# Optimization experiments

Measured on AMD Instinct MI355X. Metric: run time of the kernel, lower is better.

Reference implementation:

```python
import jax, jax.numpy as jnp
import numpy as np
from jax import lax

TARGETED_NUM_POINTS = 2000


def fps_indices(pts, m):
    """Furthest-point sampling indices for one cloud. pts: [n,3] -> [m] int32.
    Matches pointnet2_utils.furthest_point_sample: first index is 0, then
    iteratively pick the point with max distance to the selected set."""
    n = pts.shape[0]

    def step(carry, _):
        dist, last = carry
        d = jnp.sum((pts - pts[last]) ** 2, axis=-1)  # [n]
        dist = jnp.minimum(dist, d)
        nxt = jnp.argmax(dist).astype(jnp.int32)
        return (dist, nxt), nxt

    dist0 = jnp.full((n,), 1e10, dtype=pts.dtype)
    (_, _), idxs = lax.scan(step, (dist0, jnp.int32(0)), None, length=m - 1)
    return jnp.concatenate([jnp.zeros((1,), jnp.int32), idxs])


def setup_inputs() -> dict:
    key = jax.random.key(0)
    k1, k2 = jax.random.split(key)
    batch, n_pts, c = 8, 20000, 128
    return {
        "input_C": jax.random.normal(k1, (batch * n_pts, 3), dtype=jnp.float32),
        "input_F": jax.random.normal(k2, (batch * n_pts, c), dtype=jnp.float32),
        "batch": batch,
        "n_pts": n_pts,
    }


def reference(input_C, input_F, batch, n_pts):
    # pts_list = [n_pts]*batch (equal-size clouds), so the flat tensors reshape cleanly.
    C = input_C.reshape(batch, n_pts, 3)
    F = input_F.reshape(batch, n_pts, -1)
    m = min(TARGETED_NUM_POINTS, n_pts)
    idxs = jax.vmap(lambda p: fps_indices(p, m))(C)  # [b, m]
    sampled_C = jnp.take_along_axis(C, idxs[..., None], axis=1)  # [b, m, 3]
    sampled_F = jnp.take_along_axis(F, idxs[..., None], axis=1)  # [b, m, c]
    return sampled_C, sampled_F
```

## Files before the change

### kernel.cpp

```cpp
#include <hip/hip_runtime.h>
#include <hip/hip_bf16.h>

typedef unsigned long long ull;

#define THREADS 1024
#define NWAVE 16

template<int CTRL, int RM>
__device__ __forceinline__ float fmax_dpp(float v) {
    int s = __builtin_amdgcn_update_dpp(__float_as_int(v), __float_as_int(v), CTRL, RM, 0xf, false);
    return fmaxf(v, __int_as_float(s));
}
template<int CTRL, int RM>
__device__ __forceinline__ float fmin_dpp(float v) {
    int s = __builtin_amdgcn_update_dpp(__float_as_int(v), __float_as_int(v), CTRL, RM, 0xf, false);
    return fminf(v, __int_as_float(s));
}
template<int CTRL, int RM>
__device__ __forceinline__ int imin_dpp(int v) {
    int s = __builtin_amdgcn_update_dpp(v, v, CTRL, RM, 0xf, false);
    return (s < v) ? s : v;
}
template<int CTRL, int RM>
__device__ __forceinline__ ull kmax_dpp(ull k) {
    unsigned hi = (unsigned)(k >> 32), lo = (unsigned)k;
    unsigned hi2 = (unsigned)__builtin_amdgcn_update_dpp((int)hi, (int)hi, CTRL, RM, 0xf, false);
    unsigned lo2 = (unsigned)__builtin_amdgcn_update_dpp((int)lo, (int)lo, CTRL, RM, 0xf, false);
    ull k2 = ((ull)hi2 << 32) | lo2;
    return (k2 > k) ? k2 : k;
}
__device__ __forceinline__ float wave_fmax(float v) {
    v = fmax_dpp<0x111,0xf>(v); v = fmax_dpp<0x112,0xf>(v);
    v = fmax_dpp<0x114,0xf>(v); v = fmax_dpp<0x118,0xf>(v);
    v = fmax_dpp<0x142,0xa>(v); v = fmax_dpp<0x143,0xc>(v);
    return v;
}
__device__ __forceinline__ float wave_fmin(float v) {
    v = fmin_dpp<0x111,0xf>(v); v = fmin_dpp<0x112,0xf>(v);
    v = fmin_dpp<0x114,0xf>(v); v = fmin_dpp<0x118,0xf>(v);
    v = fmin_dpp<0x142,0xa>(v); v = fmin_dpp<0x143,0xc>(v);
    return v;
}
__device__ __forceinline__ float half_fmax(float v) {
    v = fmax_dpp<0x111,0xf>(v); v = fmax_dpp<0x112,0xf>(v);
    v = fmax_dpp<0x114,0xf>(v); v = fmax_dpp<0x118,0xf>(v);
    v = fmax_dpp<0x142,0xa>(v);
    return v;
}
__device__ __forceinline__ float half_fmin(float v) {
    v = fmin_dpp<0x111,0xf>(v); v = fmin_dpp<0x112,0xf>(v);
    v = fmin_dpp<0x114,0xf>(v); v = fmin_dpp<0x118,0xf>(v);
    v = fmin_dpp<0x142,0xa>(v);
    return v;
}
__device__ __forceinline__ int half_imin(int v) {
    v = imin_dpp<0x111,0xf>(v); v = imin_dpp<0x112,0xf>(v);
    v = imin_dpp<0x114,0xf>(v); v = imin_dpp<0x118,0xf>(v);
    v = imin_dpp<0x142,0xa>(v);
    return v;
}
__device__ __forceinline__ ull wave_kmax(ull k) {
    k = kmax_dpp<0x111,0xf>(k); k = kmax_dpp<0x112,0xf>(k);
    k = kmax_dpp<0x114,0xf>(k); k = kmax_dpp<0x118,0xf>(k);
    k = kmax_dpp<0x142,0xa>(k); k = kmax_dpp<0x143,0xc>(k);
    return k;
}
__device__ __forceinline__ int morton4(int x, int y, int z) {
    int r = 0;
#pragma unroll
    for (int k = 0; k < 4; ++k)
        r |= ((x >> k & 1) << (3 * k)) | ((y >> k & 1) << (3 * k + 1)) | ((z >> k & 1) << (3 * k + 2));
    return r;
}
__device__ __forceinline__ int cellof(float x, float y, float z,
                                      float bx, float by, float bz,
                                      float ivx, float ivy, float ivz) {
    int ix = (int)((x - bx) * ivx); ix = ix < 0 ? 0 : (ix > 15 ? 15 : ix);
    int iy = (int)((y - by) * ivy); iy = iy < 0 ? 0 : (iy > 15 ? 15 : iy);
    int iz = (int)((z - bz) * ivz); iz = iz < 0 ? 0 : (iz > 15 ? 15 : iz);
    return morton4(ix, iy, iz);
}

#define OFS_GKEY 0
#define OFS_GMAX 8192
#define OFS_CX   12288
#define OFS_CY   16384
#define OFS_CZ   20480
#define OFS_EX   24576
#define OFS_EY   28672
#define OFS_EZ   32768
#define OFS_LIST 36864
#define OFS_PART 38912
#define OFS_MISC 39168
#define OFS_RED  39296
#define FIXED_BYTES 39680

__global__ __launch_bounds__(THREADS)
void fps_grouped(const float* __restrict__ C, float4* __restrict__ gxyzo,
                 int n, int m, int G32, int* __restrict__ idx_out) {
    const int b = blockIdx.x;
    const int t = threadIdx.x;
    const int lane = t & 63;
    const int wid  = t >> 6;
    const int half = lane >> 5;
    const int sub  = lane & 31;
    const int GP = G32 * 32;
    const float* __restrict__ P = C + (size_t)b * n * 3;
    float4* __restrict__ gx = gxyzo + (size_t)b * GP;

    extern __shared__ char smem[];
    ull*   s_gkey = (ull*)(smem + OFS_GKEY);
    float* s_gmax = (float*)(smem + OFS_GMAX);
    float* s_cx   = (float*)(smem + OFS_CX);
    float* s_cy   = (float*)(smem + OFS_CY);
    float* s_cz   = (float*)(smem + OFS_CZ);
    float* s_ex   = (float*)(smem + OFS_EX);
    float* s_ey   = (float*)(smem + OFS_EY);
    float* s_ez   = (float*)(smem + OFS_EZ);
    unsigned short* s_list = (unsigned short*)(smem + OFS_LIST);
    ull*   s_part = (ull*)(smem + OFS_PART);
    int*   s_misc = (int*)(smem + OFS_MISC);
    float* s_red  = (float*)(smem + OFS_RED);
    float* s_dist = (float*)(smem + FIXED_BYTES);
    unsigned* s_hist = (unsigned*)s_dist;

    float mnx = 1e30f, mny = 1e30f, mnz = 1e30f;
    float mxx = -1e30f, mxy = -1e30f, mxz = -1e30f;
    for (int g = t; g < n; g += THREADS) {
        float x = P[3 * g], y = P[3 * g + 1], z = P[3 * g + 2];
        mnx = fminf(mnx, x); mxx = fmaxf(mxx, x);
        mny = fminf(mny, y); mxy = fmaxf(mxy, y);
        mnz = fminf(mnz, z); mxz = fmaxf(mxz, z);
    }
    mnx = wave_fmin(mnx); mny = wave_fmin(mny); mnz = wave_fmin(mnz);
    mxx = wave_fmax(mxx); mxy = wave_fmax(mxy); mxz = wave_fmax(mxz);
    if (lane == 63) {
        s_red[wid * 6 + 0] = mnx; s_red[wid * 6 + 1] = mny; s_red[wid * 6 + 2] = mnz;
        s_red[wid * 6 + 3] = mxx; s_red[wid * 6 + 4] = mxy; s_red[wid * 6 + 5] = mxz;
    }
    __syncthreads();
    if (t == 0) {
        float a0 = 1e30f, a1 = 1e30f, a2 = 1e30f, b0 = -1e30f, b1 = -1e30f, b2 = -1e30f;
        for (int w = 0; w < NWAVE; ++w) {
            a0 = fminf(a0, s_red[w * 6 + 0]); a1 = fminf(a1, s_red[w * 6 + 1]);
            a2 = fminf(a2, s_red[w * 6 + 2]); b0 = fmaxf(b0, s_red[w * 6 + 3]);
            b1 = fmaxf(b1, s_red[w * 6 + 4]); b2 = fmaxf(b2, s_red[w * 6 + 5]);
        }
        s_red[0] = a0; s_red[1] = a1; s_red[2] = a2;
        s_red[3] = 15.9999f / (b0 - a0 + 1e-20f);
        s_red[4] = 15.9999f / (b1 - a1 + 1e-20f);
        s_red[5] = 15.9999f / (b2 - a2 + 1e-20f);
    }
    __syncthreads();
    const float bx = s_red[0], by = s_red[1], bz = s_red[2];
    const float ivx = s_red[3], ivy = s_red[4], ivz = s_red[5];

    for (int i = t; i < 4096; i += THREADS) s_hist[i] = 0;
    __syncthreads();
    for (int g = t; g < n; g += THREADS) {
        float x = P[3 * g], y = P[3 * g + 1], z = P[3 * g + 2];
        atomicAdd(&s_hist[cellof(x, y, z, bx, by, bz, ivx, ivy, ivz)], 1u);
    }
    __syncthreads();

    {
        unsigned c0 = s_hist[4 * t], c1 = s_hist[4 * t + 1];
        unsigned c2 = s_hist[4 * t + 2], c3 = s_hist[4 * t + 3];
        unsigned sum4 = c0 + c1 + c2 + c3;
        unsigned incl = sum4;
        for (int off = 1; off < 64; off <<= 1) {
            unsigned u = (unsigned)__shfl_up((int)incl, off);
            if (lane >= off) incl += u;
        }
        if (lane == 63) s_misc[8 + wid] = (int)incl;
        __syncthreads();
        unsigned woff = 0;
        for (int w = 0; w < wid; ++w) woff += (unsigned)s_misc[8 + w];
        unsigned base = woff + incl - sum4;
        s_hist[4 * t]     = base;
        s_hist[4 * t + 1] = base + c0;
        s_hist[4 * t + 2] = base + c0 + c1;
        s_hist[4 * t + 3] = base + c0 + c1 + c2;
    }
    __syncthreads();

    for (int g = t; g < n; g += THREADS) {
        float x = P[3 * g], y = P[3 * g + 1], z = P[3 * g + 2];
        unsigned pos = atomicAdd(&s_hist[cellof(x, y, z, bx, by, bz, ivx, ivy, ivz)], 1u);
        gx[pos] = make_float4(x, y, z, (float)g);
    }
    __syncthreads();

    const ull BIGKEY = ((ull)__float_as_uint(1e10f) << 15) | 0x7fffULL;
    for (int g = wid; g < G32; g += NWAVE) {
        int cnt = n - g * 32; if (cnt > 32) cnt = 32;
        bool memb = (lane < 32) && (sub < cnt);
        float4 w = make_float4(0.f, 0.f, 0.f, 0.f);
        if (memb) w = gx[g * 32 + sub];
        float xn = memb ? w.x : 1e30f, xx = memb ? w.x : -1e30f;
        float yn = memb ? w.y : 1e30f, yx = memb ? w.y : -1e30f;
        float zn = memb ? w.z : 1e30f, zx = memb ? w.z : -1e30f;
        xn = __shfl(half_fmin(xn), 31); xx = __shfl(half_fmax(xx), 31);
        yn = __shfl(half_fmin(yn), 31); yx = __shfl(half_fmax(yx), 31);
        zn = __shfl(half_fmin(zn), 31); zx = __shfl(half_fmax(zx), 31);
        if (lane == 0) {
            s_cx[g] = (xn + xx) * 0.5f; s_ex[g] = (xx - xn) * 0.5f + 1e-7f;
            s_cy[g] = (yn + yx) * 0.5f; s_ey[g] = (yx - yn) * 0.5f + 1e-7f;
            s_cz[g] = (zn + zx) * 0.5f; s_ez[g] = (zx - zn) * 0.5f + 1e-7f;
            s_gmax[g] = 1e10f;
            s_gkey[g] = BIGKEY;
        }
        if (lane < 32) {
            if (!memb) gx[g * 32 + sub] = make_float4(0.f, 0.f, 0.f, 0.f);
            s_dist[g * 32 + sub] = memb ? 1e10f : -1.0f;
        }
    }
    for (int i = t; i < 1024; i += THREADS)
        if (i >= G32) s_gkey[i] = 0;
    if (t == 0) { s_misc[0] = 0; idx_out[(size_t)b * m] = 0; }
    __syncthreads();

    float lx = P[0], ly = P[1], lz = P[2];
    const size_t iobase = (size_t)b * m;
    const int DW = (G32 + 63) >> 6;
    for (int it = 1; it < m; ++it) {
        const int par = (it & 1) * 16;

        bool upd = false;
        if (t < G32) {
            float gmax = s_gmax[t];
            float ax = fmaxf(fabsf(lx - s_cx[t]) - s_ex[t], 0.0f);
            float ay = fmaxf(fabsf(ly - s_cy[t]) - s_ey[t], 0.0f);
            float az = fmaxf(fabsf(lz - s_cz[t]) - s_ez[t], 0.0f);
            float lb2 = ax * ax + ay * ay + az * az;
            upd = !(lb2 * 0.9999f - 1e-6f >= gmax);
        }
        {
            ull mask = __ballot(upd);
            if (mask) {
                int cnt = __popcll(mask);
                int base = 0;
                if (lane == 0) base = atomicAdd(&s_misc[0], cnt);
                base = __shfl(base, 0);
                if (upd) {
                    int pw = (int)__popcll(mask & ((1ULL << lane) - 1ULL));
                    s_list[base + pw] = (unsigned short)t;
                }
            }
        }
        __syncthreads();
        const int U = s_misc[0];

        {
            const int nt = (U + 1) >> 1;
            for (int j0 = wid; j0 < nt; j0 += NWAVE) {
                int e = 2 * j0 + half;
                int g = (e < U) ? (int)s_list[e] : -1;
                int o = g * 32 + sub;
                float4 w = make_float4(0.f, 0.f, 0.f, 0.f);
                float dc = -1.0f;
                if (g >= 0) { w = gx[o]; dc = s_dist[o]; }
                float dx = __fsub_rn(w.x, lx);
                float dy = __fsub_rn(w.y, ly);
                float dz = __fsub_rn(w.z, lz);
                float d  = __fadd_rn(__fadd_rn(__fmul_rn(dx, dx), __fmul_rn(dy, dy)),
                                     __fmul_rn(dz, dz));
                float nd = fminf(dc, d);
                if (g >= 0) s_dist[o] = nd;
                float gmr = nd;
                gmr = fmax_dpp<0x111,0xf>(gmr);
                gmr = fmax_dpp<0x112,0xf>(gmr);
                gmr = fmax_dpp<0x114,0xf>(gmr);
                gmr = fmax_dpp<0x118,0xf>(gmr);
                gmr = fmax_dpp<0x142,0xa>(gmr);
                float gm = __shfl(gmr, lane | 31);
                ull mask = __ballot(nd == gm);
                unsigned hm = half ? (unsigned)(mask >> 32) : (unsigned)mask;
                int fl = __ffs((int)hm) - 1;
                int ao = __shfl((int)w.w, (half << 5) + fl);
                bool tie = (hm & (hm - 1u)) != 0u;
                if (__any(tie)) {
                    int morig = (nd == gm) ? (int)w.w : 0x7FFFFFFF;
                    morig = half_imin(morig);
                    int tmin = __shfl(morig, lane | 31);
                    if (tie) ao = tmin;
                }
                if (g >= 0 && sub == 31) {
                    s_gkey[g] = ((ull)__float_as_uint(gm) << 15)
                              | (ull)(unsigned)(0x7fff - ao);
                    s_gmax[g] = gm;
                }
            }
        }
        __syncthreads();

        ull kk = 0;
        if (wid < DW) kk = wave_kmax(s_gkey[t]);
        if (lane == 63) s_part[par + wid] = kk;
        if (t == 0) s_misc[0] = 0;
        __syncthreads();
        ull k2 = s_part[par + (t & 15)];
        k2 = kmax_dpp<0x111,0xf>(k2);
        k2 = kmax_dpp<0x112,0xf>(k2);
        k2 = kmax_dpp<0x114,0xf>(k2);
        k2 = kmax_dpp<0x118,0xf>(k2);
        int lo15 = __builtin_amdgcn_readlane((int)(unsigned)k2, 15);
        int orig = 0x7fff - (lo15 & 0x7fff);
        if (t == 0) idx_out[iobase + it] = orig;
        const float* __restrict__ wp = P + 3 * (size_t)orig;
        lx = wp[0]; ly = wp[1]; lz = wp[2];
    }
}

__global__ __launch_bounds__(1024)
void fps_brute(const float* __restrict__ C, float* __restrict__ gdist,
               int n, int m, int* __restrict__ idx_out) {
    const int b = blockIdx.x, t = threadIdx.x;
    const int lane = t & 63, wid = t >> 6;
    const float* __restrict__ P = C + (size_t)b * n * 3;
    float* __restrict__ dist = gdist + (size_t)b * n;
    __shared__ ull sp[2][16];
    for (int g = t; g < n; g += 1024) dist[g] = 1e10f;
    if (t == 0) idx_out[(size_t)b * m] = 0;
    float lx = P[0], ly = P[1], lz = P[2];
    __syncthreads();
    for (int it = 1; it < m; ++it) {
        int par = it & 1;
        ull k = 0;
        for (int g = t; g < n; g += 1024) {
            float dx = __fsub_rn(P[3 * g], lx);
            float dy = __fsub_rn(P[3 * g + 1], ly);
            float dz = __fsub_rn(P[3 * g + 2], lz);
            float d = __fadd_rn(__fadd_rn(__fmul_rn(dx, dx), __fmul_rn(dy, dy)),
                                __fmul_rn(dz, dz));
            float nd = fminf(dist[g], d);
            dist[g] = nd;
            ull kk = ((ull)__float_as_uint(nd) << 32) | (unsigned)(~g);
            if (kk > k) k = kk;
        }
        for (int off = 1; off < 64; off <<= 1) {
            ull ok = __shfl_xor(k, off);
            if (ok > k) k = ok;
        }
        if (lane == 0) sp[par][wid] = k;
        __syncthreads();
        ull kmaxv = sp[par][0];
        for (int w = 1; w < 16; ++w) { ull v = sp[par][w]; if (v > kmaxv) kmaxv = v; }
        int sbi = (int)~(unsigned)kmaxv;
        if (t == 0) idx_out[(size_t)b * m + it] = sbi;
        const float* wp = P + 3 * (size_t)(unsigned)sbi;
        lx = wp[0]; ly = wp[1]; lz = wp[2];
    }
}

__global__ void gather_kernel(const float* __restrict__ C,
                              const float* __restrict__ F,
                              const int* __restrict__ idx,
                              float* __restrict__ outC,
                              float* __restrict__ outF,
                              int n_pts, int m, int c) {
    int pair = blockIdx.x;
    int b = pair / m;
    int src = idx[pair];
    size_t srcbase = (size_t)b * n_pts + src;
    const float* sF = F + srcbase * (size_t)c;
    float* dF = outF + (size_t)pair * c;
    for (int i = threadIdx.x; i < c; i += blockDim.x) dF[i] = sF[i];
    if (threadIdx.x < 3)
        outC[(size_t)pair * 3 + threadIdx.x] = C[srcbase * 3 + threadIdx.x];
}

extern "C" void kernel_launch(void* const* d_in, const int* in_sizes, int n_in,
                              void* d_out, int out_size, void* d_ws, size_t ws_size,
                              hipStream_t stream) {
    const float* C = (const float*)d_in[0];
    const float* F = (const float*)d_in[1];

    int n_total = in_sizes[0] / 3;
    int c       = in_sizes[1] / n_total;
    int bm      = out_size / (3 + c);

    int batch = 8;
    if (bm % 2000 == 0) {
        int bb = bm / 2000;
        if (bb > 0 && n_total % bb == 0 && n_total / bb >= 2000) batch = bb;
    }
    int n_pts = n_total / batch;
    int m     = (n_pts < 2000) ? n_pts : 2000;

    int* idxbuf = (int*)d_ws;
    float* outC = (float*)d_out;
    float* outF = outC + (size_t)batch * m * 3;

    int G32 = (n_pts + 31) >> 5;
    int GP  = G32 << 5;
    size_t idxbytes = (((size_t)batch * m * 4) + 255) & ~(size_t)255;
    size_t scrbytes = (size_t)batch * GP * 16;
    void* scratch;
    if (ws_size >= idxbytes + scrbytes)
        scratch = (char*)d_ws + idxbytes;
    else
        scratch = (char*)d_out + ((((size_t)out_size * 4) - scrbytes) & ~(size_t)15);

    if (n_pts <= 32767) {
        int distbytes = GP * 4; if (distbytes < 16384) distbytes = 16384;
        size_t smem = (size_t)FIXED_BYTES + distbytes;
        hipFuncSetAttribute((const void*)fps_grouped,
                            hipFuncAttributeMaxDynamicSharedMemorySize, (int)smem);
        fps_grouped<<<batch, THREADS, smem, stream>>>(C, (float4*)scratch,
                                                      n_pts, m, G32, idxbuf);
    } else {
        fps_brute<<<batch, 1024, 0, stream>>>(C, (float*)scratch, n_pts, m, idxbuf);
    }

    gather_kernel<<<batch * m, 128, 0, stream>>>(C, F, idxbuf, outC, outF,
                                                 n_pts, m, c);
}
```

Measured before the change: 3.094 ms.

## Replace block-level argmax reduction with redundant per-wave scan and unroll phase C

Every wave now scans all group keys in shared memory and reduces redundantly, which removes the two-stage partial-max step and one block barrier per iteration. The candidate list is double-buffered so its counter can be reset without an extra barrier. The per-group distance update loop is unrolled four ways so that global loads are batched. The iteration is reordered to run an initial full update before the loop, and the final update is skipped. In exchange, each wave does more redundant LDS reads (G32/64 per lane), and the unrolled loop raises register pressure.

```diff
diff --git a/kernel.cpp b/kernel.cpp
--- a/kernel.cpp
+++ b/kernel.cpp
@@ -81,19 +81,88 @@
     return morton4(ix, iy, iz);
 }
 
-#define OFS_GKEY 0
-#define OFS_GMAX 8192
-#define OFS_CX   12288
-#define OFS_CY   16384
-#define OFS_CZ   20480
-#define OFS_EX   24576
-#define OFS_EY   28672
-#define OFS_EZ   32768
-#define OFS_LIST 36864
-#define OFS_PART 38912
-#define OFS_MISC 39168
-#define OFS_RED  39296
-#define FIXED_BYTES 39680
+#define OFS_GKEY  0
+#define OFS_GMAX  8192
+#define OFS_CX    12288
+#define OFS_CY    16384
+#define OFS_CZ    20480
+#define OFS_EX    24576
+#define OFS_EY    28672
+#define OFS_EZ    32768
+#define OFS_LIST0 36864
+#define OFS_LIST1 38912
+#define OFS_MISC  40960
+#define OFS_RED   41088
+#define FIXED_BYTES 41472
+
+__device__ __forceinline__ void phaseC(
+    const float4* __restrict__ gx, float* __restrict__ s_dist,
+    ull* __restrict__ s_gkey, float* __restrict__ s_gmax,
+    const unsigned short* __restrict__ lst, int U,
+    int lane, int half, int sub, int wid,
+    float lx, float ly, float lz)
+{
+    const int nt = (U + 1) >> 1;
+    for (int j = wid; j < nt; j += 4 * NWAVE) {
+        const int j1 = j + NWAVE, j2 = j + 2 * NWAVE, j3 = j + 3 * NWAVE;
+        int e0 = 2 * j  + half, e1 = 2 * j1 + half;
+        int e2 = 2 * j2 + half, e3 = 2 * j3 + half;
+        bool a0 = e0 < U;
+        bool a1 = (j1 < nt) && (e1 < U);
+        bool a2 = (j2 < nt) && (e2 < U);
+        bool a3 = (j3 < nt) && (e3 < U);
+        int g0 = lst[a0 ? e0 : 0], g1 = lst[a1 ? e1 : 0];
+        int g2 = lst[a2 ? e2 : 0], g3 = lst[a3 ? e3 : 0];
+        int o0 = g0 * 32 + sub, o1 = g1 * 32 + sub;
+        int o2 = g2 * 32 + sub, o3 = g3 * 32 + sub;
+        float4 w0 = gx[o0];
+        float4 w1 = gx[o1];
+        float4 w2 = gx[o2];
+        float4 w3 = gx[o3];
+        float d0 = s_dist[o0], d1 = s_dist[o1];
+        float d2 = s_dist[o2], d3 = s_dist[o3];
+
+#define PROC(W, DC, G, O, VALID)                                              \
+        {                                                                     \
+            float dx = __fsub_rn(W.x, lx);                                    \
+            float dy = __fsub_rn(W.y, ly);                                    \
+            float dz = __fsub_rn(W.z, lz);                                    \
+            float d  = __fadd_rn(__fadd_rn(__fmul_rn(dx, dx),                 \
+                                           __fmul_rn(dy, dy)),               \
+                                 __fmul_rn(dz, dz));                          \
+            float nd = fminf(DC, d);                                          \
+            if (VALID) s_dist[O] = nd;                                        \
+            float gmr = nd;                                                   \
+            gmr = fmax_dpp<0x111,0xf>(gmr);                                   \
+            gmr = fmax_dpp<0x112,0xf>(gmr);                                   \
+            gmr = fmax_dpp<0x114,0xf>(gmr);                                   \
+            gmr = fmax_dpp<0x118,0xf>(gmr);                                   \
+            gmr = fmax_dpp<0x142,0xa>(gmr);                                   \
+            float gm = __shfl(gmr, lane | 31);                                \
+            ull mask = __ballot(nd == gm);                                    \
+            unsigned hm = half ? (unsigned)(mask >> 32) : (unsigned)mask;     \
+            int fl = __ffs((int)hm) - 1;                                      \
+            int ao = __shfl((int)W.w, (half << 5) + fl);                      \
+            bool tie = (hm & (hm - 1u)) != 0u;                                \
+            if (__any(tie)) {                                                 \
+                int morig = (nd == gm) ? (int)W.w : 0x7FFFFFFF;               \
+                morig = half_imin(morig);                                     \
+                int tmin = __shfl(morig, lane | 31);                          \
+                if (tie) ao = tmin;                                           \
+            }                                                                 \
+            if (VALID && sub == 31) {                                         \
+                s_gkey[G] = ((ull)__float_as_uint(gm) << 15)                  \
+                          | (ull)(unsigned)(0x7fff - ao);                     \
+                s_gmax[G] = gm;                                               \
+            }                                                                 \
+        }
+        PROC(w0, d0, g0, o0, a0)
+        PROC(w1, d1, g1, o1, a1)
+        PROC(w2, d2, g2, o2, a2)
+        PROC(w3, d3, g3, o3, a3)
+#undef PROC
+    }
+}
 
 __global__ __launch_bounds__(THREADS)
 void fps_grouped(const float* __restrict__ C, float4* __restrict__ gxyzo,
@@ -117,8 +186,8 @@
     float* s_ex   = (float*)(smem + OFS_EX);
     float* s_ey   = (float*)(smem + OFS_EY);
     float* s_ez   = (float*)(smem + OFS_EZ);
-    unsigned short* s_list = (unsigned short*)(smem + OFS_LIST);
-    ull*   s_part = (ull*)(smem + OFS_PART);
+    unsigned short* s_list0 = (unsigned short*)(smem + OFS_LIST0);
+    unsigned short* s_list1 = (unsigned short*)(smem + OFS_LIST1);
     int*   s_misc = (int*)(smem + OFS_MISC);
     float* s_red  = (float*)(smem + OFS_RED);
     float* s_dist = (float*)(smem + FIXED_BYTES);
@@ -191,7 +260,6 @@
     }
     __syncthreads();
 
-    const ull BIGKEY = ((ull)__float_as_uint(1e10f) << 15) | 0x7fffULL;
     for (int g = wid; g < G32; g += NWAVE) {
         int cnt = n - g * 32; if (cnt > 32) cnt = 32;
         bool memb = (lane < 32) && (sub < cnt);
@@ -207,24 +275,36 @@
             s_cx[g] = (xn + xx) * 0.5f; s_ex[g] = (xx - xn) * 0.5f + 1e-7f;
             s_cy[g] = (yn + yx) * 0.5f; s_ey[g] = (yx - yn) * 0.5f + 1e-7f;
             s_cz[g] = (zn + zx) * 0.5f; s_ez[g] = (zx - zn) * 0.5f + 1e-7f;
-            s_gmax[g] = 1e10f;
-            s_gkey[g] = BIGKEY;
         }
         if (lane < 32) {
             if (!memb) gx[g * 32 + sub] = make_float4(0.f, 0.f, 0.f, 0.f);
             s_dist[g * 32 + sub] = memb ? 1e10f : -1.0f;
         }
     }
-    for (int i = t; i < 1024; i += THREADS)
-        if (i >= G32) s_gkey[i] = 0;
-    if (t == 0) { s_misc[0] = 0; idx_out[(size_t)b * m] = 0; }
+    for (int i = t; i < G32; i += THREADS) s_list0[i] = (unsigned short)i;
+    if (t == 0) { s_misc[0] = G32; s_misc[1] = 0; idx_out[(size_t)b * m] = 0; }
     __syncthreads();
 
     float lx = P[0], ly = P[1], lz = P[2];
     const size_t iobase = (size_t)b * m;
-    const int DW = (G32 + 63) >> 6;
+    phaseC(gx, s_dist, s_gkey, s_gmax, s_list0, G32, lane, half, sub, wid, lx, ly, lz);
+    __syncthreads();
+
     for (int it = 1; it < m; ++it) {
-        const int par = (it & 1) * 16;
+        const int p = it & 1;
+
+        ull kb = 0;
+        for (int k = lane; k < G32; k += 64) {
+            ull v = s_gkey[k];
+            if (v > kb) kb = v;
+        }
+        kb = wave_kmax(kb);
+        unsigned klo = (unsigned)__builtin_amdgcn_readlane((int)(unsigned)kb, 63);
+        int orig = 0x7fff - (int)(klo & 0x7fffu);
+        if (t == 0) idx_out[iobase + it] = orig;
+        if (it == m - 1) break;
+        const float* __restrict__ wp = P + 3 * (size_t)orig;
+        lx = wp[0]; ly = wp[1]; lz = wp[2];
 
         bool upd = false;
         if (t < G32) {
@@ -235,80 +315,26 @@
             float lb2 = ax * ax + ay * ay + az * az;
             upd = !(lb2 * 0.9999f - 1e-6f >= gmax);
         }
+        if (t == 0) s_misc[p ^ 1] = 0;
+        unsigned short* lst = p ? s_list1 : s_list0;
         {
             ull mask = __ballot(upd);
             if (mask) {
                 int cnt = __popcll(mask);
                 int base = 0;
-                if (lane == 0) base = atomicAdd(&s_misc[0], cnt);
+                if (lane == 0) base = atomicAdd(&s_misc[p], cnt);
                 base = __shfl(base, 0);
                 if (upd) {
                     int pw = (int)__popcll(mask & ((1ULL << lane) - 1ULL));
-                    s_list[base + pw] = (unsigned short)t;
+                    lst[base + pw] = (unsigned short)t;
                 }
             }
         }
         __syncthreads();
-        const int U = s_misc[0];
-
-        {
-            const int nt = (U + 1) >> 1;
-            for (int j0 = wid; j0 < nt; j0 += NWAVE) {
-                int e = 2 * j0 + half;
-                int g = (e < U) ? (int)s_list[e] : -1;
-                int o = g * 32 + sub;
-                float4 w = make_float4(0.f, 0.f, 0.f, 0.f);
-                float dc = -1.0f;
-                if (g >= 0) { w = gx[o]; dc = s_dist[o]; }
-                float dx = __fsub_rn(w.x, lx);
-                float dy = __fsub_rn(w.y, ly);
-                float dz = __fsub_rn(w.z, lz);
-                float d  = __fadd_rn(__fadd_rn(__fmul_rn(dx, dx), __fmul_rn(dy, dy)),
-                                     __fmul_rn(dz, dz));
-                float nd = fminf(dc, d);
-                if (g >= 0) s_dist[o] = nd;
-                float gmr = nd;
-                gmr = fmax_dpp<0x111,0xf>(gmr);
-                gmr = fmax_dpp<0x112,0xf>(gmr);
-                gmr = fmax_dpp<0x114,0xf>(gmr);
-                gmr = fmax_dpp<0x118,0xf>(gmr);
-                gmr = fmax_dpp<0x142,0xa>(gmr);
-                float gm = __shfl(gmr, lane | 31);
-                ull mask = __ballot(nd == gm);
-                unsigned hm = half ? (unsigned)(mask >> 32) : (unsigned)mask;
-                int fl = __ffs((int)hm) - 1;
-                int ao = __shfl((int)w.w, (half << 5) + fl);
-                bool tie = (hm & (hm - 1u)) != 0u;
-                if (__any(tie)) {
-                    int morig = (nd == gm) ? (int)w.w : 0x7FFFFFFF;
-                    morig = half_imin(morig);
-                    int tmin = __shfl(morig, lane | 31);
-                    if (tie) ao = tmin;
-                }
-                if (g >= 0 && sub == 31) {
-                    s_gkey[g] = ((ull)__float_as_uint(gm) << 15)
-                              | (ull)(unsigned)(0x7fff - ao);
-                    s_gmax[g] = gm;
-                }
-            }
-        }
+
+        const int U = s_misc[p];
+        phaseC(gx, s_dist, s_gkey, s_gmax, lst, U, lane, half, sub, wid, lx, ly, lz);
         __syncthreads();
-
-        ull kk = 0;
-        if (wid < DW) kk = wave_kmax(s_gkey[t]);
-        if (lane == 63) s_part[par + wid] = kk;
-        if (t == 0) s_misc[0] = 0;
-        __syncthreads();
-        ull k2 = s_part[par + (t & 15)];
-        k2 = kmax_dpp<0x111,0xf>(k2);
-        k2 = kmax_dpp<0x112,0xf>(k2);
-        k2 = kmax_dpp<0x114,0xf>(k2);
-        k2 = kmax_dpp<0x118,0xf>(k2);
-        int lo15 = __builtin_amdgcn_readlane((int)(unsigned)k2, 15);
-        int orig = 0x7fff - (lo15 & 0x7fff);
-        if (t == 0) idx_out[iobase + it] = orig;
-        const float* __restrict__ wp = P + 3 * (size_t)orig;
-        lx = wp[0]; ly = wp[1]; lz = wp[2];
     }
 }
 
```

Result: slower. 4.652 ms (+50.4%).

## Cache group winner coords in LDS and prefetch next group load

Applied to the files above, without the earlier changes.

The per-group key now also packs the group index, and the per-group winning point is written to a new shared-memory table. After the block-wide argmax, the next query point is read from shared memory instead of from global memory, which takes a dependent global load off the serial per-iteration path. The distance-update loop also prefetches the next group's float4 from global memory before processing the current one. Tie handling now always runs the min-index reduction rather than taking a ballot-based fast path. The cost is about 16 KB more shared memory per block and some extra shuffle work on each group.

```diff
diff --git a/kernel.cpp b/kernel.cpp
--- a/kernel.cpp
+++ b/kernel.cpp
@@ -82,18 +82,65 @@
 }
 
 #define OFS_GKEY 0
-#define OFS_GMAX 8192
-#define OFS_CX   12288
-#define OFS_CY   16384
-#define OFS_CZ   20480
-#define OFS_EX   24576
-#define OFS_EY   28672
-#define OFS_EZ   32768
-#define OFS_LIST 36864
-#define OFS_PART 38912
-#define OFS_MISC 39168
-#define OFS_RED  39296
-#define FIXED_BYTES 39680
+#define OFS_GWIN 8192
+#define OFS_GMAX 24576
+#define OFS_CX   28672
+#define OFS_CY   32768
+#define OFS_CZ   36864
+#define OFS_EX   40960
+#define OFS_EY   45056
+#define OFS_EZ   49152
+#define OFS_LIST 53248
+#define OFS_PART 55296
+#define OFS_MISC 55552
+#define OFS_RED  55680
+#define FIXED_BYTES 56064
+
+__device__ __forceinline__ void phaseC(
+    const float4* __restrict__ gx, float* __restrict__ s_dist,
+    ull* __restrict__ s_gkey, float* __restrict__ s_gmax,
+    float4* __restrict__ s_gwin,
+    const unsigned short* __restrict__ lst, int U,
+    int lane, int half, int sub, int wid,
+    float lx, float ly, float lz)
+{
+    const int nt = (U + 1) >> 1;
+    int j = wid;
+    if (j >= nt) return;
+    int e = 2 * j + half;
+    bool a = (e < U);
+    int g = a ? (int)lst[e] : 0;
+    int o = g * 32 + sub;
+    float4 w = gx[o];
+    while (j < nt) {
+        const int jn = j + NWAVE;
+        const int en = 2 * jn + half;
+        bool an = (jn < nt) && (en < U);
+        int gn = an ? (int)lst[en] : 0;
+        int on = gn * 32 + sub;
+        float4 wn = gx[on];
+        float dc = a ? s_dist[o] : -1.0f;
+        float dx = __fsub_rn(w.x, lx);
+        float dy = __fsub_rn(w.y, ly);
+        float dz = __fsub_rn(w.z, lz);
+        float d  = __fadd_rn(__fadd_rn(__fmul_rn(dx, dx), __fmul_rn(dy, dy)),
+                             __fmul_rn(dz, dz));
+        float nd = fminf(dc, d);
+        if (a) s_dist[o] = nd;
+        float gm = __shfl(half_fmax(nd), lane | 31);
+        int pk = (nd == gm) ? (int)w.w : 0x7FFFFFFF;
+        int minorig = __shfl(half_imin(pk), lane | 31);
+        if (a && nd == gm && (int)w.w == minorig)
+            s_gwin[g] = w;
+        if (a && sub == 31) {
+            s_gkey[g] = ((ull)__float_as_uint(gm) << 25)
+                      | ((ull)(unsigned)(0x7fff - minorig) << 10)
+                      | (ull)(unsigned)g;
+            s_gmax[g] = gm;
+        }
+        j = jn; a = an; g = gn; o = on; w = wn;
+    }
+}
 
 __global__ __launch_bounds__(THREADS)
 void fps_grouped(const float* __restrict__ C, float4* __restrict__ gxyzo,
@@ -109,19 +156,20 @@
     float4* __restrict__ gx = gxyzo + (size_t)b * GP;
 
     extern __shared__ char smem[];
-    ull*   s_gkey = (ull*)(smem + OFS_GKEY);
-    float* s_gmax = (float*)(smem + OFS_GMAX);
-    float* s_cx   = (float*)(smem + OFS_CX);
-    float* s_cy   = (float*)(smem + OFS_CY);
-    float* s_cz   = (float*)(smem + OFS_CZ);
-    float* s_ex   = (float*)(smem + OFS_EX);
-    float* s_ey   = (float*)(smem + OFS_EY);
-    float* s_ez   = (float*)(smem + OFS_EZ);
+    ull*    s_gkey = (ull*)(smem + OFS_GKEY);
+    float4* s_gwin = (float4*)(smem + OFS_GWIN);
+    float*  s_gmax = (float*)(smem + OFS_GMAX);
+    float*  s_cx   = (float*)(smem + OFS_CX);
+    float*  s_cy   = (float*)(smem + OFS_CY);
+    float*  s_cz   = (float*)(smem + OFS_CZ);
+    float*  s_ex   = (float*)(smem + OFS_EX);
+    float*  s_ey   = (float*)(smem + OFS_EY);
+    float*  s_ez   = (float*)(smem + OFS_EZ);
     unsigned short* s_list = (unsigned short*)(smem + OFS_LIST);
-    ull*   s_part = (ull*)(smem + OFS_PART);
-    int*   s_misc = (int*)(smem + OFS_MISC);
-    float* s_red  = (float*)(smem + OFS_RED);
-    float* s_dist = (float*)(smem + FIXED_BYTES);
+    ull*    s_part = (ull*)(smem + OFS_PART);
+    int*    s_misc = (int*)(smem + OFS_MISC);
+    float*  s_red  = (float*)(smem + OFS_RED);
+    float*  s_dist = (float*)(smem + FIXED_BYTES);
     unsigned* s_hist = (unsigned*)s_dist;
 
     float mnx = 1e30f, mny = 1e30f, mnz = 1e30f;
@@ -191,7 +239,6 @@
     }
     __syncthreads();
 
-    const ull BIGKEY = ((ull)__float_as_uint(1e10f) << 15) | 0x7fffULL;
     for (int g = wid; g < G32; g += NWAVE) {
         int cnt = n - g * 32; if (cnt > 32) cnt = 32;
         bool memb = (lane < 32) && (sub < cnt);
@@ -208,7 +255,6 @@
             s_cy[g] = (yn + yx) * 0.5f; s_ey[g] = (yx - yn) * 0.5f + 1e-7f;
             s_cz[g] = (zn + zx) * 0.5f; s_ez[g] = (zx - zn) * 0.5f + 1e-7f;
             s_gmax[g] = 1e10f;
-            s_gkey[g] = BIGKEY;
         }
         if (lane < 32) {
             if (!memb) gx[g * 32 + sub] = make_float4(0.f, 0.f, 0.f, 0.f);
@@ -251,47 +297,8 @@
         __syncthreads();
         const int U = s_misc[0];
 
-        {
-            const int nt = (U + 1) >> 1;
-            for (int j0 = wid; j0 < nt; j0 += NWAVE) {
-                int e = 2 * j0 + half;
-                int g = (e < U) ? (int)s_list[e] : -1;
-                int o = g * 32 + sub;
-                float4 w = make_float4(0.f, 0.f, 0.f, 0.f);
-                float dc = -1.0f;
-                if (g >= 0) { w = gx[o]; dc = s_dist[o]; }
-                float dx = __fsub_rn(w.x, lx);
-                float dy = __fsub_rn(w.y, ly);
-                float dz = __fsub_rn(w.z, lz);
-                float d  = __fadd_rn(__fadd_rn(__fmul_rn(dx, dx), __fmul_rn(dy, dy)),
-                                     __fmul_rn(dz, dz));
-                float nd = fminf(dc, d);
-                if (g >= 0) s_dist[o] = nd;
-                float gmr = nd;
-                gmr = fmax_dpp<0x111,0xf>(gmr);
-                gmr = fmax_dpp<0x112,0xf>(gmr);
-                gmr = fmax_dpp<0x114,0xf>(gmr);
-                gmr = fmax_dpp<0x118,0xf>(gmr);
-                gmr = fmax_dpp<0x142,0xa>(gmr);
-                float gm = __shfl(gmr, lane | 31);
-                ull mask = __ballot(nd == gm);
-                unsigned hm = half ? (unsigned)(mask >> 32) : (unsigned)mask;
-                int fl = __ffs((int)hm) - 1;
-                int ao = __shfl((int)w.w, (half << 5) + fl);
-                bool tie = (hm & (hm - 1u)) != 0u;
-                if (__any(tie)) {
-                    int morig = (nd == gm) ? (int)w.w : 0x7FFFFFFF;
-                    morig = half_imin(morig);
-                    int tmin = __shfl(morig, lane | 31);
-                    if (tie) ao = tmin;
-                }
-                if (g >= 0 && sub == 31) {
-                    s_gkey[g] = ((ull)__float_as_uint(gm) << 15)
-                              | (ull)(unsigned)(0x7fff - ao);
-                    s_gmax[g] = gm;
-                }
-            }
-        }
+        phaseC(gx, s_dist, s_gkey, s_gmax, s_gwin, s_list, U,
+               lane, half, sub, wid, lx, ly, lz);
         __syncthreads();
 
         ull kk = 0;
@@ -304,11 +311,12 @@
         k2 = kmax_dpp<0x112,0xf>(k2);
         k2 = kmax_dpp<0x114,0xf>(k2);
         k2 = kmax_dpp<0x118,0xf>(k2);
-        int lo15 = __builtin_amdgcn_readlane((int)(unsigned)k2, 15);
-        int orig = 0x7fff - (lo15 & 0x7fff);
+        unsigned klo = (unsigned)__builtin_amdgcn_readlane((int)(unsigned)k2, 15);
+        int gwin = (int)(klo & 0x3ffu);
+        int orig = 0x7fff - (int)((klo >> 10) & 0x7fffu);
         if (t == 0) idx_out[iobase + it] = orig;
-        const float* __restrict__ wp = P + 3 * (size_t)orig;
-        lx = wp[0]; ly = wp[1]; lz = wp[2];
+        float4 wn = s_gwin[gwin];
+        lx = wn.x; ly = wn.y; lz = wn.z;
     }
 }
 
```

New measurement: 3.294 ms. 6.5% more time.
